# Kernel optimization log

Measured on AMD Instinct MI355X. Metric: run time of the kernel, lower is better.

Reference implementation:

```python
import jax, jax.numpy as jnp
import numpy as np
from jax import lax

B, P, S, H, F, V, O = 32, 24, 48, 512, 64, 50000, 16
EPS = 1e-5


def _lstm_scan(inputs, Wih, Whh, b):
    # inputs: [T, B, D]; PyTorch gate order i, f, g, o
    def step(carry, xt):
        h, c = carry
        g = xt @ Wih.T + h @ Whh.T + b
        i, f, gg, o = jnp.split(g, 4, axis=-1)
        c = jax.nn.sigmoid(f) * c + jax.nn.sigmoid(i) * jnp.tanh(gg)
        h = jax.nn.sigmoid(o) * jnp.tanh(c)
        return (h, c), h
    b_ = inputs.shape[1]
    h0 = jnp.zeros((b_, Whh.shape[1]), inputs.dtype)
    _, hs = lax.scan(step, (h0, h0), inputs)
    return hs


def setup_inputs() -> dict:
    key = jax.random.key(0)
    ks = jax.random.split(key, 16)
    x = jax.random.randint(ks[0], (B, P, S), 0, V)
    lens = jnp.sort(jax.random.randint(ks[1], (B,), 1, P + 1))[::-1]
    lens = lens.at[0].set(P)  # pack_padded: sorted desc, max len == P
    tok_len = jax.random.randint(ks[2], (B, P), 1, S + 1)
    tok_len = tok_len * (jnp.arange(P)[None, :] < lens[:, None])
    x_mask = jnp.arange(S)[None, None, :] >= tok_len[:, :, None]  # True = pad
    x_feature = jax.random.normal(ks[3], (B, P, S, F), dtype=jnp.float32)
    emb = jax.random.normal(ks[4], (V, H), dtype=jnp.float32) * 0.02
    w_attn = jax.random.normal(ks[5], (H,), dtype=jnp.float32) * 0.02
    b_attn = jnp.zeros((), jnp.float32)
    D = H + F
    s = 1.0 / np.sqrt(H)
    u = lambda k, sh: jax.random.uniform(k, sh, jnp.float32, -s, s)
    Wih_f, Whh_f = u(ks[6], (4 * H, D)), u(ks[7], (4 * H, H))
    bih_f, bhh_f = u(ks[8], (4 * H,)), u(ks[9], (4 * H,))
    Wih_b, Whh_b = u(ks[10], (4 * H, D)), u(ks[11], (4 * H, H))
    bih_b, bhh_b = u(ks[12], (4 * H,)), u(ks[13], (4 * H,))
    Wfc = u(ks[14], (O, 2 * H))
    bfc = jnp.zeros((O,), jnp.float32)
    gamma = jnp.ones((O,), jnp.float32)
    beta = jnp.zeros((O,), jnp.float32)
    return {"x": x, "x_mask": x_mask, "x_feature": x_feature,
            "sentences_len": lens, "clause": 0, "cls": 0,
            "emb": emb, "w_attn": w_attn, "b_attn": b_attn,
            "Wih_f": Wih_f, "Whh_f": Whh_f, "bih_f": bih_f, "bhh_f": bhh_f,
            "Wih_b": Wih_b, "Whh_b": Whh_b, "bih_b": bih_b, "bhh_b": bhh_b,
            "Wfc": Wfc, "bfc": bfc, "gamma": gamma, "beta": beta}


def reference(x, x_mask, x_feature, sentences_len, clause, cls,
              emb, w_attn, b_attn,
              Wih_f, Whh_f, bih_f, bhh_f,
              Wih_b, Whh_b, bih_b, bhh_b,
              Wfc, bfc, gamma, beta):
    # --- per-sentence embed + linear self-attention + masked sum pooling ---
    e = emb[x]                                             # [B,P,S,H]
    scores = jnp.einsum('bpsh,h->bps', e, w_attn) + b_attn  # [B,P,S]
    scores = jnp.where(x_mask, -1e30, scores)
    alpha = jax.nn.softmax(scores, axis=-1)
    alpha = jnp.where(x_mask, 0.0, alpha)                  # zeros empty sents; relu(softmax)=softmax
    valid = (~x_mask).astype(e.dtype)
    weighted = e * alpha[..., None]
    cat = jnp.concatenate([weighted, x_feature], axis=-1) * valid[..., None]
    rep = cat.sum(axis=2)                                  # [B,P,H+F]
    seq = jnp.transpose(rep, (1, 0, 2))                    # time-major [P,B,H+F]

    # --- packed bidirectional LSTM (per-sequence reversal for bwd dir) ---
    t = jnp.arange(P)[:, None]                             # [P,1]
    lens = sentences_len[None, :]                          # [1,B]
    valid_t = (t < lens)                                   # [P,B]
    h_fwd = _lstm_scan(seq, Wih_f, Whh_f, bih_f + bhh_f)
    rev_idx = jnp.clip(lens - 1 - t, 0)                    # [P,B]
    rev_in = jnp.take_along_axis(seq, rev_idx[..., None], axis=0)
    h_bwd_rev = _lstm_scan(rev_in, Wih_b, Whh_b, bih_b + bhh_b)
    h_bwd = jnp.take_along_axis(h_bwd_rev, rev_idx[..., None], axis=0)
    out_seq = jnp.concatenate([h_fwd, h_bwd], axis=-1) * valid_t[..., None]  # pad_packed zeros

    # --- tail: last timestep, fc, train-mode BN, relu, log_softmax(dim=0) ---
    last = out_seq[-1]                                     # [B,2H]
    z = jnp.reshape(last.T, (B, 2 * H))                    # faithful transpose+view quirk
    y = z @ Wfc.T + bfc                                    # [B,O]
    mean = y.mean(axis=0)
    var = y.var(axis=0)                                    # biased, as torch BN normalization
    y = gamma * (y - mean) / jnp.sqrt(var + EPS) + beta
    y = jax.nn.relu(y)
    return jax.nn.log_softmax(y, axis=0)
```

## Files before the change

### kernel.cpp

```cpp
#include <hip/hip_runtime.h>
#include <math.h>

#define BB_ 32
#define PP_ 24
#define SS_ 48
#define HH_ 512
#define FF_ 64
#define DD_ 576
#define G4_ 2048

typedef __attribute__((ext_vector_type(8))) short short8;
typedef __attribute__((ext_vector_type(4))) float f32x4;

__device__ __forceinline__ float sigf(float x) { return 1.f / (1.f + expf(-x)); }

__device__ __forceinline__ unsigned short f2bf(float f) {
    unsigned int u = __float_as_uint(f);
    u += 0x7FFFu + ((u >> 16) & 1u);
    return (unsigned short)(u >> 16);
}

__global__ void __launch_bounds__(256) prep_attn_kernel(
        const int* __restrict__ x, const unsigned int* __restrict__ maskw,
        const float* __restrict__ x_feature, const float* __restrict__ emb,
        const float* __restrict__ w_attn, const float* __restrict__ b_attn,
        const float* __restrict__ Whh, unsigned short* __restrict__ Bf,
        const float* __restrict__ Wih, unsigned short* __restrict__ Wbf,
        float* __restrict__ AfA, int* __restrict__ flags,
        float* __restrict__ seq, unsigned short* __restrict__ seqb)
{
    int blk = blockIdx.x, tid = threadIdx.x;
    if (blk < 768) {
        __shared__ float sc_s[SS_], alpha_s[SS_];
        __shared__ int vtok[SS_], vpos[SS_];
        __shared__ int nv_s, s_u8, s_f32;
        __shared__ int idx_s[SS_];
        __shared__ unsigned char msk_s[SS_];
        if (tid == 0) { s_u8 = 0; s_f32 = 0; }
        __syncthreads();
        int u8 = 0, f32 = 0;
        for (int i = tid; i < 9216; i += 256) {
            unsigned int w = maskw[i];
            if (w == 0x3F800000u) f32 = 1;
            else if (w > 1u) u8 = 1;
        }
        if (u8) s_u8 = 1;
        if (f32) s_f32 = 1;
        __syncthreads();
        int mode = s_f32 ? 2 : (s_u8 ? 1 : 0);
        int bp = blk, b = bp / PP_, p = bp % PP_;
        if (tid < SS_) {
            size_t i = (size_t)bp * SS_ + tid;
            idx_s[tid] = x[i];
            unsigned char mv;
            if (mode == 1)      mv = ((const unsigned char*)maskw)[i];
            else if (mode == 2) mv = (((const float*)maskw)[i] != 0.f);
            else                mv = (((const int*)maskw)[i] != 0);
            msk_s[tid] = mv;
        }
        __syncthreads();
        if (tid == 0) {
            int nv = 0;
            for (int s = 0; s < SS_; ++s)
                if (!msk_s[s]) { vtok[nv] = idx_s[s]; vpos[nv] = s; ++nv; }
            nv_s = nv;
        }
        __syncthreads();
        int nv = nv_s;
        int wave = tid >> 6, lane = tid & 63;
        float4 wa0 = ((const float4*)w_attn)[lane];
        float4 wa1 = ((const float4*)w_attn)[64 + lane];
        for (int j = wave; j < nv; j += 4) {
            const float4* er4 = (const float4*)(emb + (size_t)vtok[j] * HH_);
            float4 v0 = er4[lane], v1 = er4[64 + lane];
            float acc = v0.x * wa0.x + v0.y * wa0.y + v0.z * wa0.z + v0.w * wa0.w
                      + v1.x * wa1.x + v1.y * wa1.y + v1.z * wa1.z + v1.w * wa1.w;
            #pragma unroll
            for (int off = 32; off > 0; off >>= 1) acc += __shfl_down(acc, off, 64);
            if (lane == 0) sc_s[j] = acc + b_attn[0];
        }
        __syncthreads();
        if (tid == 0) {
            float m = -3.4e38f;
            for (int j = 0; j < nv; ++j) if (sc_s[j] > m) m = sc_s[j];
            float sum = 0.f;
            for (int j = 0; j < nv; ++j) { float a = expf(sc_s[j] - m); alpha_s[j] = a; sum += a; }
            float inv = (nv > 0) ? (1.f / sum) : 0.f;
            for (int j = 0; j < nv; ++j) alpha_s[j] *= inv;
        }
        __syncthreads();
        float acc0 = 0.f, acc1 = 0.f;
        for (int j = 0; j < nv; ++j) {
            float a = alpha_s[j];
            const float* er = emb + (size_t)vtok[j] * HH_;
            acc0 += a * er[tid];
            acc1 += a * er[tid + 256];
        }
        float* orow = seq + ((size_t)p * BB_ + b) * DD_;
        unsigned short* ob = seqb + ((size_t)p * BB_ + b) * DD_;
        orow[tid] = acc0;
        orow[tid + 256] = acc1;
        ob[tid] = f2bf(acc0);
        ob[tid + 256] = f2bf(acc1);
        if (tid < FF_) {
            float accF = 0.f;
            for (int j = 0; j < nv; ++j)
                accF += x_feature[((size_t)bp * SS_ + vpos[j]) * FF_ + tid];
            orow[HH_ + tid] = accF;
            ob[HH_ + tid] = f2bf(accF);
        }
    } else if (blk < 1280) {
        int idx = (blk - 768) * 256 + tid;
        int lane = idx & 63;
        int ks = (idx >> 6) & 15;
        int ti = (idx >> 10) & 1;
        int nb = idx >> 11;
        int c = lane & 15, q = lane >> 4;
        int nrow = (ti * 2 + (c >> 3)) * HH_ + nb * 8 + (c & 7);
        int k0 = ks * 32 + q * 8;
        const float* src = Whh + (size_t)nrow * HH_ + k0;
        unsigned int w0 = (unsigned int)f2bf(src[0]) | ((unsigned int)f2bf(src[1]) << 16);
        unsigned int w1 = (unsigned int)f2bf(src[2]) | ((unsigned int)f2bf(src[3]) << 16);
        unsigned int w2 = (unsigned int)f2bf(src[4]) | ((unsigned int)f2bf(src[5]) << 16);
        unsigned int w3 = (unsigned int)f2bf(src[6]) | ((unsigned int)f2bf(src[7]) << 16);
        *(uint4*)(Bf + (size_t)idx * 8) = make_uint4(w0, w1, w2, w3);
    } else if (blk < 2432) {
        int i = (blk - 1280) * 256 + tid;
        float4 v = ((const float4*)Wih)[i];
        ushort4 o;
        o.x = f2bf(v.x); o.y = f2bf(v.y); o.z = f2bf(v.z); o.w = f2bf(v.w);
        ((ushort4*)Wbf)[i] = o;
    } else if (blk < 2464) {
        int idx = (blk - 2432) * 256 + tid;
        if (idx < 8192) AfA[idx] = 0.f;
    } else {
        if (tid < 64) flags[tid] = 0;
    }
}

__global__ void __launch_bounds__(256) in_gates_mfma_kernel(
        const unsigned short* __restrict__ Ab,
        const unsigned short* __restrict__ Wbf,
        const float* __restrict__ bih,
        const float* __restrict__ bhh,
        float* __restrict__ Cout)
{
    int tid = threadIdx.x, lane = tid & 63, w = tid >> 6;
    int m0 = blockIdx.y * 16;
    int nb = blockIdx.x * 128 + w * 32;
    int c = lane & 15, q = lane >> 4;
    const unsigned short* Ap  = Ab  + (size_t)(m0 + c) * DD_ + q * 8;
    const unsigned short* Bp0 = Wbf + (size_t)(nb + c) * DD_ + q * 8;
    const unsigned short* Bp1 = Bp0 + 16 * DD_;
    f32x4 acc0 = {0.f, 0.f, 0.f, 0.f}, acc1 = {0.f, 0.f, 0.f, 0.f};
    for (int k = 0; k < DD_; k += 32) {
        short8 a  = *(const short8*)(Ap  + k);
        short8 b0 = *(const short8*)(Bp0 + k);
        short8 b1 = *(const short8*)(Bp1 + k);
        acc0 = __builtin_amdgcn_mfma_f32_16x16x32_bf16(a, b0, acc0, 0, 0, 0);
        acc1 = __builtin_amdgcn_mfma_f32_16x16x32_bf16(a, b1, acc1, 0, 0, 0);
    }
    #pragma unroll
    for (int r = 0; r < 4; ++r) {
        int m = m0 + q * 4 + r;
        int n0 = nb + c, n1 = nb + 16 + c;
        Cout[(size_t)m * G4_ + n0] = acc0[r] + bih[n0] + bhh[n0];
        Cout[(size_t)m * G4_ + n1] = acc1[r] + bih[n1] + bhh[n1];
    }
}

__global__ void __launch_bounds__(256) lstm_bwd_kernel(
        unsigned short* __restrict__ AfA, unsigned short* __restrict__ AfB,
        float* __restrict__ hbuf, const float* __restrict__ Ain,
        const unsigned short* __restrict__ Bfrag, int* __restrict__ flags,
        const float* __restrict__ seq, const int* __restrict__ lens,
        const float* __restrict__ Wih_b, const float* __restrict__ bih_b,
        const float* __restrict__ bhh_b, float* __restrict__ hbw)
{
    __shared__ float smem[19040];
    int tid = threadIdx.x;
    if (blockIdx.x < 64) {
        float* gl = smem;
        int lane = tid & 63, wv = tid >> 6;
        int mt = wv & 1, ti = wv >> 1;
        int nb = blockIdx.x;
        const short8* Bp = (const short8*)Bfrag + (((size_t)nb * 2 + ti) * 16) * 64 + lane;
        short8 bfr[16];
        #pragma unroll
        for (int ks = 0; ks < 16; ++ks) bfr[ks] = Bp[ks * 64];
        int c = lane & 15, q = lane >> 4;
        int g = ti * 2 + (c >> 3), ul = c & 7;
        int b2s = tid >> 1, hf2 = tid & 1;
        float creg[4] = {0.f, 0.f, 0.f, 0.f};
        const float* ainp = Ain + (size_t)(mt * 16 + q * 4) * G4_ + g * HH_ + nb * 8 + ul;
        float ainx[4], ainn[4];
        #pragma unroll
        for (int r = 0; r < 4; ++r) ainx[r] = ainp[(size_t)r * G4_];
        for (int t = 0; t < PP_; ++t) {
            if (t + 1 < PP_) {
                const float* np = ainp + (size_t)(t + 1) * BB_ * G4_;
                #pragma unroll
                for (int r = 0; r < 4; ++r) ainn[r] = np[(size_t)r * G4_];
            }
            const unsigned short* Af = (t & 1) ? AfB : AfA;
            unsigned short* An       = (t & 1) ? AfA : AfB;
            const unsigned long long* Ap64 =
                (const unsigned long long*)Af + ((size_t)(mt * 16) * 64 + lane) * 2;
            short8 a[16];
            #pragma unroll
            for (int ks = 0; ks < 16; ++ks) {
                unsigned long long lo = __hip_atomic_load(Ap64 + (size_t)ks * 128,
                        __ATOMIC_RELAXED, __HIP_MEMORY_SCOPE_AGENT);
                unsigned long long hi = __hip_atomic_load(Ap64 + (size_t)ks * 128 + 1,
                        __ATOMIC_RELAXED, __HIP_MEMORY_SCOPE_AGENT);
                union { unsigned long long u[2]; short8 s; } cv;
                cv.u[0] = lo; cv.u[1] = hi;
                a[ks] = cv.s;
            }
            f32x4 acA = {0.f,0.f,0.f,0.f}, acB = {0.f,0.f,0.f,0.f};
            f32x4 acC = {0.f,0.f,0.f,0.f}, acD = {0.f,0.f,0.f,0.f};
            #pragma unroll
            for (int ks = 0; ks < 16; ks += 4) {
                acA = __builtin_amdgcn_mfma_f32_16x16x32_bf16(a[ks],     bfr[ks],     acA, 0, 0, 0);
                acB = __builtin_amdgcn_mfma_f32_16x16x32_bf16(a[ks + 1], bfr[ks + 1], acB, 0, 0, 0);
                acC = __builtin_amdgcn_mfma_f32_16x16x32_bf16(a[ks + 2], bfr[ks + 2], acC, 0, 0, 0);
                acD = __builtin_amdgcn_mfma_f32_16x16x32_bf16(a[ks + 3], bfr[ks + 3], acD, 0, 0, 0);
            }
            #pragma unroll
            for (int r = 0; r < 4; ++r) {
                float v = (acA[r] + acB[r]) + (acC[r] + acD[r]) + ainx[r];
                v = (g == 2) ? tanhf(v) : sigf(v);
                gl[(g * 8 + ul) * 33 + (mt * 16 + q * 4 + r)] = v;
            }
            __syncthreads();
            if (t == PP_ - 1) {
                if (tid < 64) {
                    #pragma unroll
                    for (int uu = 0; uu < 4; ++uu) {
                        int u = hf2 * 4 + uu;
                        float iv = gl[(     u) * 33 + b2s];
                        float fv = gl[( 8 + u) * 33 + b2s];
                        float gv = gl[(16 + u) * 33 + b2s];
                        float ov = gl[(24 + u) * 33 + b2s];
                        creg[uu] = fv * creg[uu] + iv * gv;
                        hbuf[(size_t)b2s * HH_ + nb * 8 + u] = ov * tanhf(creg[uu]);
                    }
                }
            } else {
                if (tid < 64) {
                    float h4[4];
                    #pragma unroll
                    for (int uu = 0; uu < 4; ++uu) {
                        int u = hf2 * 4 + uu;
                        float iv = gl[(     u) * 33 + b2s];
                        float fv = gl[( 8 + u) * 33 + b2s];
                        float gv = gl[(16 + u) * 33 + b2s];
                        float ov = gl[(24 + u) * 33 + b2s];
                        creg[uu] = fv * creg[uu] + iv * gv;
                        h4[uu] = ov * tanhf(creg[uu]);
                    }
                    unsigned long long vv = (unsigned long long)f2bf(h4[0])
                                          | ((unsigned long long)f2bf(h4[1]) << 16)
                                          | ((unsigned long long)f2bf(h4[2]) << 32)
                                          | ((unsigned long long)f2bf(h4[3]) << 48);
                    size_t ub = ((((size_t)(b2s >> 4)) * 16 + (nb >> 2)) * 64
                                 + ((b2s & 15) + 16 * (nb & 3))) * 8 + hf2 * 4;
                    __hip_atomic_store((unsigned long long*)(AfA + (An - AfA) + ub), vv,
                                       __ATOMIC_RELAXED, __HIP_MEMORY_SCOPE_AGENT);
                    asm volatile("s_waitcnt vmcnt(0)" ::: "memory");
                    if (tid == 0)
                        __hip_atomic_store(&flags[nb], t + 1,
                                           __ATOMIC_RELAXED, __HIP_MEMORY_SCOPE_AGENT);
                    int target = t + 1;
                    while (true) {
                        int fvv = __hip_atomic_load(&flags[tid],
                                __ATOMIC_RELAXED, __HIP_MEMORY_SCOPE_AGENT);
                        if (__all(fvv >= target)) break;
                        __builtin_amdgcn_s_sleep(1);
                    }
                }
                __syncthreads();
            }
            #pragma unroll
            for (int r = 0; r < 4; ++r) ainx[r] = ainn[r];
        }
    } else {
        float* xsT = smem;
        int* pl = (int*)(smem + 19008);
        int blk2 = blockIdx.x - 64;
        if (tid < BB_) pl[tid] = lens[tid] - 1;
        __syncthreads();
        for (int idx = tid; idx < BB_ * DD_; idx += 256) {
            int b2 = idx / DD_;
            int k = idx - b2 * DD_;
            xsT[k * 33 + b2] = seq[((size_t)pl[b2] * BB_ + b2) * DD_ + k];
        }
        __syncthreads();
        int b = tid & 31, ul = tid >> 5;
        int u = blk2 * 8 + ul;
        const float* wi = Wih_b + (size_t)u * DD_;
        const float* wg = Wih_b + (size_t)(2 * HH_ + u) * DD_;
        const float* wo = Wih_b + (size_t)(3 * HH_ + u) * DD_;
        float gi = 0.f, gg = 0.f, go = 0.f;
        #pragma unroll 4
        for (int k = 0; k < DD_; k += 4) {
            float4 w1 = *(const float4*)(wi + k);
            float4 w2 = *(const float4*)(wg + k);
            float4 w3 = *(const float4*)(wo + k);
            float x0 = xsT[(k + 0) * 33 + b];
            float x1 = xsT[(k + 1) * 33 + b];
            float x2 = xsT[(k + 2) * 33 + b];
            float x3 = xsT[(k + 3) * 33 + b];
            gi += w1.x * x0 + w1.y * x1 + w1.z * x2 + w1.w * x3;
            gg += w2.x * x0 + w2.y * x1 + w2.z * x2 + w2.w * x3;
            go += w3.x * x0 + w3.y * x1 + w3.z * x2 + w3.w * x3;
        }
        gi += bih_b[u] + bhh_b[u];
        gg += bih_b[2 * HH_ + u] + bhh_b[2 * HH_ + u];
        go += bih_b[3 * HH_ + u] + bhh_b[3 * HH_ + u];
        float cc = sigf(gi) * tanhf(gg);
        hbw[(size_t)b * HH_ + u] = sigf(go) * tanhf(cc);
    }
}

__global__ void __launch_bounds__(1024) head_fused_kernel(
        const float* __restrict__ hf, const float* __restrict__ hbwd,
        const int* __restrict__ lens,
        const float* __restrict__ Wfc, const float* __restrict__ bfc,
        const float* __restrict__ gamma, const float* __restrict__ beta,
        float* __restrict__ out)
{
    __shared__ float tileL[32 * 1024];
    __shared__ float lmask[BB_];
    __shared__ float part[1024];
    __shared__ float ys[16][33];
    __shared__ float cstat[16];
    int tid = threadIdx.x;
    if (tid < BB_) lmask[tid] = (lens[tid] == PP_) ? 1.f : 0.f;
    __syncthreads();
    for (int j = tid; j < 32 * 1024; j += 1024) {
        int bb = j >> 10, col = j & 1023;
        float v = (col < HH_) ? hf[(size_t)bb * HH_ + col]
                              : hbwd[(size_t)bb * HH_ + col - HH_];
        tileL[j] = v * lmask[bb];
    }
    __syncthreads();
    int outi = tid & 511, half = tid >> 9;
    int i = outi >> 4, o = outi & 15;
    const float* wrow = Wfc + (size_t)o * 1024;
    float acc = 0.f;
    for (int q = 0; q < 32; ++q) {
        int j = i * 32 + q;
        #pragma unroll
        for (int bb2 = 0; bb2 < 16; ++bb2) {
            int bb = half * 16 + bb2;
            acc += tileL[bb * 1024 + j] * wrow[q * 32 + bb];
        }
    }
    part[tid] = acc;
    __syncthreads();
    if (tid < 512) ys[o][i] = part[tid] + part[tid + 512] + bfc[o];
    __syncthreads();
    if (tid < 16) {
        float mean = 0.f;
        for (int ii = 0; ii < 32; ++ii) mean += ys[tid][ii];
        mean *= (1.f / 32.f);
        float var = 0.f;
        for (int ii = 0; ii < 32; ++ii) { float d = ys[tid][ii] - mean; var += d * d; }
        var *= (1.f / 32.f);
        float inv = 1.f / sqrtf(var + 1e-5f);
        float gmm = gamma[tid], bt = beta[tid];
        float mx = -3.4e38f;
        for (int ii = 0; ii < 32; ++ii) {
            float v = gmm * (ys[tid][ii] - mean) * inv + bt;
            v = fmaxf(v, 0.f);
            ys[tid][ii] = v;
            mx = fmaxf(mx, v);
        }
        float s = 0.f;
        for (int ii = 0; ii < 32; ++ii) s += expf(ys[tid][ii] - mx);
        cstat[tid] = mx + logf(s);
    }
    __syncthreads();
    if (tid < 512) out[tid] = ys[o][i] - cstat[o];
}

extern "C" void kernel_launch(void* const* d_in, const int* in_sizes, int n_in,
                              void* d_out, int out_size, void* d_ws, size_t ws_size,
                              hipStream_t stream) {
    const int* x            = (const int*)d_in[0];
    const void* xm          = d_in[1];
    const float* x_feature  = (const float*)d_in[2];
    const int* lens         = (const int*)d_in[3];
    const float* emb    = (const float*)d_in[6];
    const float* w_attn = (const float*)d_in[7];
    const float* b_attn = (const float*)d_in[8];
    const float* Wih_f  = (const float*)d_in[9];
    const float* Whh_f  = (const float*)d_in[10];
    const float* bih_f  = (const float*)d_in[11];
    const float* bhh_f  = (const float*)d_in[12];
    const float* Wih_b  = (const float*)d_in[13];
    const float* bih_b  = (const float*)d_in[15];
    const float* bhh_b  = (const float*)d_in[16];
    const float* Wfc    = (const float*)d_in[17];
    const float* bfc    = (const float*)d_in[18];
    const float* gamma  = (const float*)d_in[19];
    const float* beta   = (const float*)d_in[20];

    float* ws    = (float*)d_ws;
    float* seq   = ws;
    float* Ain   = seq + (size_t)PP_ * BB_ * DD_;
    float* hb    = Ain + (size_t)PP_ * BB_ * G4_;
    float* hbuf  = hb + (size_t)BB_ * HH_;
    float* AfA   = hbuf + (size_t)BB_ * HH_;
    float* AfB   = AfA + 8192;
    float* Bfrag = AfB + 8192;
    float* Wbf   = Bfrag + 524288;
    int*  flags  = (int*)(Wbf + 589824);
    unsigned short* seqb = (unsigned short*)(Wbf + 589824 + 16);

    float* outp = (float*)d_out;

    prep_attn_kernel<<<dim3(2465), dim3(256), 0, stream>>>(
        x, (const unsigned int*)xm, x_feature, emb, w_attn, b_attn,
        Whh_f, (unsigned short*)Bfrag, Wih_f, (unsigned short*)Wbf,
        AfA, flags, seq, seqb);
    in_gates_mfma_kernel<<<dim3(16, 48), dim3(256), 0, stream>>>(
        seqb, (const unsigned short*)Wbf, bih_f, bhh_f, Ain);
    lstm_bwd_kernel<<<dim3(128), dim3(256), 0, stream>>>(
        (unsigned short*)AfA, (unsigned short*)AfB, hbuf, Ain,
        (const unsigned short*)Bfrag, flags,
        seq, lens, Wih_b, bih_b, bhh_b, hb);
    head_fused_kernel<<<dim3(1), dim3(1024), 0, stream>>>(
        hbuf, hb, lens, Wfc, bfc, gamma, beta, outp);
}
```

Baseline: 444.0 us.

## Replace global barrier with per-chunk flag polling in backward LSTM recurrence

The grid-wide spin barrier after each timestep is replaced. Each wave now polls producer flags and loads each K-chunk of the hidden state as soon as its four producer blocks have published, so the MMA inputs arrive incrementally instead of after all 64 blocks finish. The trailing __syncthreads is dropped and the next step's input-gate prefetch moves inline. This aims to cut barrier latency on the serial recurrence, at the cost of more polling traffic. Removing the block sync also risks the shared gate buffer being overwritten before it is consumed.

```diff
diff --git a/kernel.cpp b/kernel.cpp
--- a/kernel.cpp
+++ b/kernel.cpp
@@ -169,7 +169,7 @@
     }
 }
 
-__global__ void __launch_bounds__(256) lstm_bwd_kernel(
+__global__ void __launch_bounds__(256, 1) lstm_bwd_kernel(
         unsigned short* __restrict__ AfA, unsigned short* __restrict__ AfB,
         float* __restrict__ hbuf, const float* __restrict__ Ain,
         const unsigned short* __restrict__ Bfrag, int* __restrict__ flags,
@@ -193,29 +193,57 @@
         int b2s = tid >> 1, hf2 = tid & 1;
         float creg[4] = {0.f, 0.f, 0.f, 0.f};
         const float* ainp = Ain + (size_t)(mt * 16 + q * 4) * G4_ + g * HH_ + nb * 8 + ul;
-        float ainx[4], ainn[4];
-        #pragma unroll
-        for (int r = 0; r < 4; ++r) ainx[r] = ainp[(size_t)r * G4_];
         for (int t = 0; t < PP_; ++t) {
-            if (t + 1 < PP_) {
-                const float* np = ainp + (size_t)(t + 1) * BB_ * G4_;
+            float ainx[4];
+            {
+                const float* ap = ainp + (size_t)t * BB_ * G4_;
                 #pragma unroll
-                for (int r = 0; r < 4; ++r) ainn[r] = np[(size_t)r * G4_];
+                for (int r = 0; r < 4; ++r) ainx[r] = ap[(size_t)r * G4_];
             }
             const unsigned short* Af = (t & 1) ? AfB : AfA;
             unsigned short* An       = (t & 1) ? AfA : AfB;
             const unsigned long long* Ap64 =
                 (const unsigned long long*)Af + ((size_t)(mt * 16) * 64 + lane) * 2;
             short8 a[16];
-            #pragma unroll
-            for (int ks = 0; ks < 16; ++ks) {
-                unsigned long long lo = __hip_atomic_load(Ap64 + (size_t)ks * 128,
-                        __ATOMIC_RELAXED, __HIP_MEMORY_SCOPE_AGENT);
-                unsigned long long hi = __hip_atomic_load(Ap64 + (size_t)ks * 128 + 1,
-                        __ATOMIC_RELAXED, __HIP_MEMORY_SCOPE_AGENT);
-                union { unsigned long long u[2]; short8 s; } cv;
-                cv.u[0] = lo; cv.u[1] = hi;
-                a[ks] = cv.s;
+            if (t == 0) {
+                #pragma unroll
+                for (int ks = 0; ks < 16; ++ks) {
+                    unsigned long long lo = __hip_atomic_load(Ap64 + (size_t)ks * 128,
+                            __ATOMIC_RELAXED, __HIP_MEMORY_SCOPE_AGENT);
+                    unsigned long long hi = __hip_atomic_load(Ap64 + (size_t)ks * 128 + 1,
+                            __ATOMIC_RELAXED, __HIP_MEMORY_SCOPE_AGENT);
+                    union { unsigned long long u[2]; short8 s; } cv;
+                    cv.u[0] = lo; cv.u[1] = hi;
+                    a[ks] = cv.s;
+                }
+            } else {
+                unsigned int got = 0;
+                while (got != 0xFFFFu) {
+                    int fv = __hip_atomic_load(&flags[lane],
+                            __ATOMIC_RELAXED, __HIP_MEMORY_SCOPE_AGENT);
+                    unsigned long long bal = __ballot(fv >= t);
+                    unsigned int rdy = 0;
+                    #pragma unroll
+                    for (int ks = 0; ks < 16; ++ks)
+                        if (((bal >> (ks * 4)) & 0xFull) == 0xFull) rdy |= 1u << ks;
+                    unsigned int news = rdy & ~got;
+                    #pragma unroll
+                    for (int ks = 0; ks < 16; ++ks) {
+                        if (news & (1u << ks)) {
+                            unsigned long long lo = __hip_atomic_load(
+                                    Ap64 + (size_t)ks * 128,
+                                    __ATOMIC_RELAXED, __HIP_MEMORY_SCOPE_AGENT);
+                            unsigned long long hi = __hip_atomic_load(
+                                    Ap64 + (size_t)ks * 128 + 1,
+                                    __ATOMIC_RELAXED, __HIP_MEMORY_SCOPE_AGENT);
+                            union { unsigned long long u[2]; short8 s; } cv;
+                            cv.u[0] = lo; cv.u[1] = hi;
+                            a[ks] = cv.s;
+                        }
+                    }
+                    got |= news;
+                    if (got != 0xFFFFu) __builtin_amdgcn_s_sleep(1);
+                }
             }
             f32x4 acA = {0.f,0.f,0.f,0.f}, acB = {0.f,0.f,0.f,0.f};
             f32x4 acC = {0.f,0.f,0.f,0.f}, acD = {0.f,0.f,0.f,0.f};
@@ -265,24 +293,14 @@
                                           | ((unsigned long long)f2bf(h4[3]) << 48);
                     size_t ub = ((((size_t)(b2s >> 4)) * 16 + (nb >> 2)) * 64
                                  + ((b2s & 15) + 16 * (nb & 3))) * 8 + hf2 * 4;
-                    __hip_atomic_store((unsigned long long*)(AfA + (An - AfA) + ub), vv,
+                    __hip_atomic_store((unsigned long long*)(An + ub), vv,
                                        __ATOMIC_RELAXED, __HIP_MEMORY_SCOPE_AGENT);
                     asm volatile("s_waitcnt vmcnt(0)" ::: "memory");
                     if (tid == 0)
                         __hip_atomic_store(&flags[nb], t + 1,
                                            __ATOMIC_RELAXED, __HIP_MEMORY_SCOPE_AGENT);
-                    int target = t + 1;
-                    while (true) {
-                        int fvv = __hip_atomic_load(&flags[tid],
-                                __ATOMIC_RELAXED, __HIP_MEMORY_SCOPE_AGENT);
-                        if (__all(fvv >= target)) break;
-                        __builtin_amdgcn_s_sleep(1);
-                    }
                 }
-                __syncthreads();
             }
-            #pragma unroll
-            for (int r = 0; r < 4; ++r) ainx[r] = ainn[r];
         }
     } else {
         float* xsT = smem;
```

Result: no change. 445.1 us (+0.2%).

## Per-wave flag sync and shuffle-based LSTM cell update in forward recurrence

Applied to the files above, without the earlier changes.

Reorders the Whh fragment layout so each MFMA tile holds all four gates for four hidden units, which lets the cell update run entirely in registers via wave shuffles instead of going through an LDS gate buffer and a block-wide barrier. Cross-block synchronisation moves from one flag per block, with a single wave spinning, to one flag per wave (256 flags), and each wave waits only on the flags of its own batch half before reading h. The B fragments move from registers into LDS, and the input-gate loads are no longer prefetched one step ahead. The aim is to remove __syncthreads and the serial single-wave cell update from the per-step critical path, at the cost of more flag polling traffic and LDS reads inside the MFMA loop.

```diff
diff --git a/kernel.cpp b/kernel.cpp
--- a/kernel.cpp
+++ b/kernel.cpp
@@ -116,7 +116,7 @@
         int ti = (idx >> 10) & 1;
         int nb = idx >> 11;
         int c = lane & 15, q = lane >> 4;
-        int nrow = (ti * 2 + (c >> 3)) * HH_ + nb * 8 + (c & 7);
+        int nrow = (c >> 2) * HH_ + nb * 8 + ti * 4 + (c & 3);
         int k0 = ks * 32 + q * 8;
         const float* src = Whh + (size_t)nrow * HH_ + k0;
         unsigned int w0 = (unsigned int)f2bf(src[0]) | ((unsigned int)f2bf(src[1]) << 16);
@@ -134,7 +134,7 @@
         int idx = (blk - 2432) * 256 + tid;
         if (idx < 8192) AfA[idx] = 0.f;
     } else {
-        if (tid < 64) flags[tid] = 0;
+        flags[tid] = 0;
     }
 }
 
@@ -169,7 +169,7 @@
     }
 }
 
-__global__ void __launch_bounds__(256) lstm_bwd_kernel(
+__global__ void __launch_bounds__(256, 1) lstm_bwd_kernel(
         unsigned short* __restrict__ AfA, unsigned short* __restrict__ AfB,
         float* __restrict__ hbuf, const float* __restrict__ Ain,
         const unsigned short* __restrict__ Bfrag, int* __restrict__ flags,
@@ -177,35 +177,48 @@
         const float* __restrict__ Wih_b, const float* __restrict__ bih_b,
         const float* __restrict__ bhh_b, float* __restrict__ hbw)
 {
-    __shared__ float smem[19040];
+    __shared__ __align__(16) float smem[19040];
     int tid = threadIdx.x;
     if (blockIdx.x < 64) {
-        float* gl = smem;
         int lane = tid & 63, wv = tid >> 6;
         int mt = wv & 1, ti = wv >> 1;
         int nb = blockIdx.x;
-        const short8* Bp = (const short8*)Bfrag + (((size_t)nb * 2 + ti) * 16) * 64 + lane;
-        short8 bfr[16];
-        #pragma unroll
-        for (int ks = 0; ks < 16; ++ks) bfr[ks] = Bp[ks * 64];
         int c = lane & 15, q = lane >> 4;
-        int g = ti * 2 + (c >> 3), ul = c & 7;
-        int b2s = tid >> 1, hf2 = tid & 1;
+        int g = c >> 2, ul = c & 3;
+        short8* lsb = (short8*)smem + (size_t)wv * 1024 + lane;
+        {
+            const short8* Bg = (const short8*)Bfrag
+                             + ((size_t)(nb * 2 + ti) * 16) * 64 + lane;
+            #pragma unroll
+            for (int ks = 0; ks < 16; ++ks) lsb[ks * 64] = Bg[ks * 64];
+        }
+        int fid = mt * 128 + nb * 2 + ti;
+        int fb  = mt * 128;
+        int lsrc = lane & 51;
+        const float* ainp = Ain + (size_t)(mt * 16 + q * 4) * G4_
+                          + g * HH_ + nb * 8 + ti * 4 + ul;
         float creg[4] = {0.f, 0.f, 0.f, 0.f};
-        const float* ainp = Ain + (size_t)(mt * 16 + q * 4) * G4_ + g * HH_ + nb * 8 + ul;
-        float ainx[4], ainn[4];
-        #pragma unroll
-        for (int r = 0; r < 4; ++r) ainx[r] = ainp[(size_t)r * G4_];
         for (int t = 0; t < PP_; ++t) {
-            if (t + 1 < PP_) {
-                const float* np = ainp + (size_t)(t + 1) * BB_ * G4_;
+            float ainx[4];
+            {
+                const float* ap = ainp + (size_t)t * BB_ * G4_;
                 #pragma unroll
-                for (int r = 0; r < 4; ++r) ainn[r] = np[(size_t)r * G4_];
+                for (int r = 0; r < 4; ++r) ainx[r] = ap[(size_t)r * G4_];
+            }
+            if (t > 0) {
+                while (true) {
+                    int f0 = __hip_atomic_load(&flags[fb + lane],
+                            __ATOMIC_RELAXED, __HIP_MEMORY_SCOPE_AGENT);
+                    int f1 = __hip_atomic_load(&flags[fb + 64 + lane],
+                            __ATOMIC_RELAXED, __HIP_MEMORY_SCOPE_AGENT);
+                    if (__all(f0 >= t && f1 >= t)) break;
+                    __builtin_amdgcn_s_sleep(1);
+                }
             }
             const unsigned short* Af = (t & 1) ? AfB : AfA;
             unsigned short* An       = (t & 1) ? AfA : AfB;
             const unsigned long long* Ap64 =
-                (const unsigned long long*)Af + ((size_t)(mt * 16) * 64 + lane) * 2;
+                (const unsigned long long*)Af + (size_t)mt * 2048 + lane * 2;
             short8 a[16];
             #pragma unroll
             for (int ks = 0; ks < 16; ++ks) {
@@ -217,72 +230,63 @@
                 cv.u[0] = lo; cv.u[1] = hi;
                 a[ks] = cv.s;
             }
-            f32x4 acA = {0.f,0.f,0.f,0.f}, acB = {0.f,0.f,0.f,0.f};
-            f32x4 acC = {0.f,0.f,0.f,0.f}, acD = {0.f,0.f,0.f,0.f};
+            f32x4 ac0 = {0.f,0.f,0.f,0.f}, ac1 = {0.f,0.f,0.f,0.f};
+            f32x4 ac2 = {0.f,0.f,0.f,0.f}, ac3 = {0.f,0.f,0.f,0.f};
             #pragma unroll
             for (int ks = 0; ks < 16; ks += 4) {
-                acA = __builtin_amdgcn_mfma_f32_16x16x32_bf16(a[ks],     bfr[ks],     acA, 0, 0, 0);
-                acB = __builtin_amdgcn_mfma_f32_16x16x32_bf16(a[ks + 1], bfr[ks + 1], acB, 0, 0, 0);
-                acC = __builtin_amdgcn_mfma_f32_16x16x32_bf16(a[ks + 2], bfr[ks + 2], acC, 0, 0, 0);
-                acD = __builtin_amdgcn_mfma_f32_16x16x32_bf16(a[ks + 3], bfr[ks + 3], acD, 0, 0, 0);
-            }
+                ac0 = __builtin_amdgcn_mfma_f32_16x16x32_bf16(a[ks],     lsb[(ks    ) * 64], ac0, 0, 0, 0);
+                ac1 = __builtin_amdgcn_mfma_f32_16x16x32_bf16(a[ks + 1], lsb[(ks + 1) * 64], ac1, 0, 0, 0);
+                ac2 = __builtin_amdgcn_mfma_f32_16x16x32_bf16(a[ks + 2], lsb[(ks + 2) * 64], ac2, 0, 0, 0);
+                ac3 = __builtin_amdgcn_mfma_f32_16x16x32_bf16(a[ks + 3], lsb[(ks + 3) * 64], ac3, 0, 0, 0);
+            }
+            float vr[4];
             #pragma unroll
             for (int r = 0; r < 4; ++r) {
-                float v = (acA[r] + acB[r]) + (acC[r] + acD[r]) + ainx[r];
-                v = (g == 2) ? tanhf(v) : sigf(v);
-                gl[(g * 8 + ul) * 33 + (mt * 16 + q * 4 + r)] = v;
-            }
-            __syncthreads();
+                float xx = (ac0[r] + ac1[r]) + (ac2[r] + ac3[r]) + ainx[r];
+                float y  = (g == 2) ? (xx + xx) : xx;
+                float s  = 1.f / (1.f + expf(-y));
+                vr[r] = (g == 2) ? (s + s - 1.f) : s;
+            }
+            float ovsel = 0.f;
+            #pragma unroll
+            for (int r = 0; r < 4; ++r) {
+                float iv = __shfl(vr[r], lsrc,      64);
+                float fv = __shfl(vr[r], lsrc | 4,  64);
+                float gv = __shfl(vr[r], lsrc | 8,  64);
+                float ov = __shfl(vr[r], lsrc | 12, 64);
+                creg[r] = fv * creg[r] + iv * gv;
+                ovsel = (r == g) ? ov : ovsel;
+            }
+            float cg = (g == 0) ? creg[0] : (g == 1) ? creg[1]
+                     : (g == 2) ? creg[2] : creg[3];
+            float s2 = 1.f / (1.f + expf(-2.f * cg));
+            float hg = ovsel * (s2 + s2 - 1.f);
+            float h0 = __shfl(hg, (lane & 60),     64);
+            float h1 = __shfl(hg, (lane & 60) | 1, 64);
+            float h2 = __shfl(hg, (lane & 60) | 2, 64);
+            float h3 = __shfl(hg, (lane & 60) | 3, 64);
+            int b = mt * 16 + q * 4 + g;
             if (t == PP_ - 1) {
-                if (tid < 64) {
-                    #pragma unroll
-                    for (int uu = 0; uu < 4; ++uu) {
-                        int u = hf2 * 4 + uu;
-                        float iv = gl[(     u) * 33 + b2s];
-                        float fv = gl[( 8 + u) * 33 + b2s];
-                        float gv = gl[(16 + u) * 33 + b2s];
-                        float ov = gl[(24 + u) * 33 + b2s];
-                        creg[uu] = fv * creg[uu] + iv * gv;
-                        hbuf[(size_t)b2s * HH_ + nb * 8 + u] = ov * tanhf(creg[uu]);
-                    }
+                if (ul == 0) {
+                    *(float4*)(hbuf + (size_t)b * HH_ + nb * 8 + ti * 4) =
+                        make_float4(h0, h1, h2, h3);
                 }
             } else {
-                if (tid < 64) {
-                    float h4[4];
-                    #pragma unroll
-                    for (int uu = 0; uu < 4; ++uu) {
-                        int u = hf2 * 4 + uu;
-                        float iv = gl[(     u) * 33 + b2s];
-                        float fv = gl[( 8 + u) * 33 + b2s];
-                        float gv = gl[(16 + u) * 33 + b2s];
-                        float ov = gl[(24 + u) * 33 + b2s];
-                        creg[uu] = fv * creg[uu] + iv * gv;
-                        h4[uu] = ov * tanhf(creg[uu]);
-                    }
-                    unsigned long long vv = (unsigned long long)f2bf(h4[0])
-                                          | ((unsigned long long)f2bf(h4[1]) << 16)
-                                          | ((unsigned long long)f2bf(h4[2]) << 32)
-                                          | ((unsigned long long)f2bf(h4[3]) << 48);
-                    size_t ub = ((((size_t)(b2s >> 4)) * 16 + (nb >> 2)) * 64
-                                 + ((b2s & 15) + 16 * (nb & 3))) * 8 + hf2 * 4;
-                    __hip_atomic_store((unsigned long long*)(AfA + (An - AfA) + ub), vv,
+                if (ul == 0) {
+                    unsigned long long vv = (unsigned long long)f2bf(h0)
+                                          | ((unsigned long long)f2bf(h1) << 16)
+                                          | ((unsigned long long)f2bf(h2) << 32)
+                                          | ((unsigned long long)f2bf(h3) << 48);
+                    size_t ui = ((size_t)(mt * 16 + (nb >> 2)) * 64
+                                 + (q * 4 + g) + 16 * (nb & 3)) * 2 + ti;
+                    __hip_atomic_store((unsigned long long*)An + ui, vv,
                                        __ATOMIC_RELAXED, __HIP_MEMORY_SCOPE_AGENT);
-                    asm volatile("s_waitcnt vmcnt(0)" ::: "memory");
-                    if (tid == 0)
-                        __hip_atomic_store(&flags[nb], t + 1,
-                                           __ATOMIC_RELAXED, __HIP_MEMORY_SCOPE_AGENT);
-                    int target = t + 1;
-                    while (true) {
-                        int fvv = __hip_atomic_load(&flags[tid],
-                                __ATOMIC_RELAXED, __HIP_MEMORY_SCOPE_AGENT);
-                        if (__all(fvv >= target)) break;
-                        __builtin_amdgcn_s_sleep(1);
-                    }
                 }
-                __syncthreads();
-            }
-            #pragma unroll
-            for (int r = 0; r < 4; ++r) ainx[r] = ainn[r];
+                asm volatile("s_waitcnt vmcnt(0)" ::: "memory");
+                if (lane == 0)
+                    __hip_atomic_store(&flags[fid], t + 1,
+                                       __ATOMIC_RELAXED, __HIP_MEMORY_SCOPE_AGENT);
+            }
         }
     } else {
         float* xsT = smem;
@@ -417,7 +421,7 @@
     float* Bfrag = AfB + 8192;
     float* Wbf   = Bfrag + 524288;
     int*  flags  = (int*)(Wbf + 589824);
-    unsigned short* seqb = (unsigned short*)(Wbf + 589824 + 16);
+    unsigned short* seqb = (unsigned short*)(Wbf + 589824 + 256);
 
     float* outp = (float*)d_out;
 
```

Result: slower. 453.2 us (+2.1%).

## Replace flag barrier with per-element step-tagged hidden state in persistent LSTM

Applied to the files above, without the earlier changes.

The recurrent LSTM kernel no longer uses a global flag array and all-blocks spin barrier each timestep. Every bf16 hidden value is now stored with a 16-bit timestep tag in a 32-bit word, and consumers poll their own A-fragment words until all tags match the current step. Cell updates are spread across all 256 threads instead of 64, and the gate buffer is double-buffered in shared memory to drop the trailing syncthreads. This trades the barrier round trip for twice the hidden-state traffic and repeated polling loads.

```diff
diff --git a/kernel.cpp b/kernel.cpp
--- a/kernel.cpp
+++ b/kernel.cpp
@@ -26,7 +26,7 @@
         const float* __restrict__ w_attn, const float* __restrict__ b_attn,
         const float* __restrict__ Whh, unsigned short* __restrict__ Bf,
         const float* __restrict__ Wih, unsigned short* __restrict__ Wbf,
-        float* __restrict__ AfA, int* __restrict__ flags,
+        unsigned int* __restrict__ AfAt,
         float* __restrict__ seq, unsigned short* __restrict__ seqb)
 {
     int blk = blockIdx.x, tid = threadIdx.x;
@@ -130,11 +130,9 @@
         ushort4 o;
         o.x = f2bf(v.x); o.y = f2bf(v.y); o.z = f2bf(v.z); o.w = f2bf(v.w);
         ((ushort4*)Wbf)[i] = o;
-    } else if (blk < 2464) {
+    } else {
         int idx = (blk - 2432) * 256 + tid;
-        if (idx < 8192) AfA[idx] = 0.f;
-    } else {
-        if (tid < 64) flags[tid] = 0;
+        ((uint4*)AfAt)[idx] = make_uint4(0u, 0u, 0u, 0u);
     }
 }
 
@@ -169,15 +167,15 @@
     }
 }
 
-__global__ void __launch_bounds__(256) lstm_bwd_kernel(
-        unsigned short* __restrict__ AfA, unsigned short* __restrict__ AfB,
+__global__ void __launch_bounds__(256, 1) lstm_bwd_kernel(
+        unsigned int* __restrict__ AfAt, unsigned int* __restrict__ AfBt,
         float* __restrict__ hbuf, const float* __restrict__ Ain,
-        const unsigned short* __restrict__ Bfrag, int* __restrict__ flags,
+        const unsigned short* __restrict__ Bfrag,
         const float* __restrict__ seq, const int* __restrict__ lens,
         const float* __restrict__ Wih_b, const float* __restrict__ bih_b,
         const float* __restrict__ bhh_b, float* __restrict__ hbw)
 {
-    __shared__ float smem[19040];
+    __shared__ __align__(16) float smem[19040];
     int tid = threadIdx.x;
     if (blockIdx.x < 64) {
         float* gl = smem;
@@ -190,32 +188,60 @@
         for (int ks = 0; ks < 16; ++ks) bfr[ks] = Bp[ks * 64];
         int c = lane & 15, q = lane >> 4;
         int g = ti * 2 + (c >> 3), ul = c & 7;
-        int b2s = tid >> 1, hf2 = tid & 1;
-        float creg[4] = {0.f, 0.f, 0.f, 0.f};
-        const float* ainp = Ain + (size_t)(mt * 16 + q * 4) * G4_ + g * HH_ + nb * 8 + ul;
-        float ainx[4], ainn[4];
-        #pragma unroll
-        for (int r = 0; r < 4; ++r) ainx[r] = ainp[(size_t)r * G4_];
+        int eb = tid >> 3, eu = tid & 7;
+        float creg = 0.f;
+        size_t eidx = ((((size_t)(eb >> 4)) * 16 + (nb >> 2)) * 64
+                       + ((eb & 15) + 16 * (nb & 3))) * 8 + eu;
+        const float* ainp = Ain + (size_t)(mt * 16 + q * 4) * G4_
+                          + g * HH_ + nb * 8 + ul;
         for (int t = 0; t < PP_; ++t) {
-            if (t + 1 < PP_) {
-                const float* np = ainp + (size_t)(t + 1) * BB_ * G4_;
+            float ainx[4];
+            {
+                const float* ap = ainp + (size_t)t * BB_ * G4_;
                 #pragma unroll
-                for (int r = 0; r < 4; ++r) ainn[r] = np[(size_t)r * G4_];
-            }
-            const unsigned short* Af = (t & 1) ? AfB : AfA;
-            unsigned short* An       = (t & 1) ? AfA : AfB;
-            const unsigned long long* Ap64 =
-                (const unsigned long long*)Af + ((size_t)(mt * 16) * 64 + lane) * 2;
+                for (int r = 0; r < 4; ++r) ainx[r] = ap[(size_t)r * G4_];
+            }
+            unsigned tgt = (unsigned)t;
+            const unsigned long long* Bas =
+                (const unsigned long long*)((t & 1) ? AfBt : AfAt)
+                + (size_t)mt * 4096 + lane * 4;
+            while (true) {
+                unsigned ok = 1u;
+                #pragma unroll
+                for (int ks = 0; ks < 16; ++ks) {
+                    unsigned long long d = __hip_atomic_load(Bas + (size_t)ks * 256,
+                            __ATOMIC_RELAXED, __HIP_MEMORY_SCOPE_AGENT);
+                    ok &= (((unsigned)d & 0xFFFFu) == tgt)
+                        & (((unsigned)(d >> 32) & 0xFFFFu) == tgt);
+                }
+                if (__all(ok)) break;
+                __builtin_amdgcn_s_sleep(1);
+            }
             short8 a[16];
-            #pragma unroll
-            for (int ks = 0; ks < 16; ++ks) {
-                unsigned long long lo = __hip_atomic_load(Ap64 + (size_t)ks * 128,
-                        __ATOMIC_RELAXED, __HIP_MEMORY_SCOPE_AGENT);
-                unsigned long long hi = __hip_atomic_load(Ap64 + (size_t)ks * 128 + 1,
-                        __ATOMIC_RELAXED, __HIP_MEMORY_SCOPE_AGENT);
-                union { unsigned long long u[2]; short8 s; } cv;
-                cv.u[0] = lo; cv.u[1] = hi;
-                a[ks] = cv.s;
+            while (true) {
+                unsigned ok = 1u;
+                #pragma unroll
+                for (int ks = 0; ks < 16; ++ks) {
+                    const unsigned long long* p = Bas + (size_t)ks * 256;
+                    unsigned long long d0 = __hip_atomic_load(p,
+                            __ATOMIC_RELAXED, __HIP_MEMORY_SCOPE_AGENT);
+                    unsigned long long d1 = __hip_atomic_load(p + 1,
+                            __ATOMIC_RELAXED, __HIP_MEMORY_SCOPE_AGENT);
+                    unsigned long long d2 = __hip_atomic_load(p + 2,
+                            __ATOMIC_RELAXED, __HIP_MEMORY_SCOPE_AGENT);
+                    unsigned long long d3 = __hip_atomic_load(p + 3,
+                            __ATOMIC_RELAXED, __HIP_MEMORY_SCOPE_AGENT);
+                    ok &= (((unsigned)d0 & 0xFFFFu) == tgt) & (((unsigned)(d0 >> 32) & 0xFFFFu) == tgt)
+                        & (((unsigned)d1 & 0xFFFFu) == tgt) & (((unsigned)(d1 >> 32) & 0xFFFFu) == tgt)
+                        & (((unsigned)d2 & 0xFFFFu) == tgt) & (((unsigned)(d2 >> 32) & 0xFFFFu) == tgt)
+                        & (((unsigned)d3 & 0xFFFFu) == tgt) & (((unsigned)(d3 >> 32) & 0xFFFFu) == tgt);
+                    a[ks][0] = (short)(d0 >> 16); a[ks][1] = (short)(d0 >> 48);
+                    a[ks][2] = (short)(d1 >> 16); a[ks][3] = (short)(d1 >> 48);
+                    a[ks][4] = (short)(d2 >> 16); a[ks][5] = (short)(d2 >> 48);
+                    a[ks][6] = (short)(d3 >> 16); a[ks][7] = (short)(d3 >> 48);
+                }
+                if (__all(ok)) break;
+                __builtin_amdgcn_s_sleep(1);
             }
             f32x4 acA = {0.f,0.f,0.f,0.f}, acB = {0.f,0.f,0.f,0.f};
             f32x4 acC = {0.f,0.f,0.f,0.f}, acD = {0.f,0.f,0.f,0.f};
@@ -226,63 +252,28 @@
                 acC = __builtin_amdgcn_mfma_f32_16x16x32_bf16(a[ks + 2], bfr[ks + 2], acC, 0, 0, 0);
                 acD = __builtin_amdgcn_mfma_f32_16x16x32_bf16(a[ks + 3], bfr[ks + 3], acD, 0, 0, 0);
             }
+            float* gls = gl + (t & 1) * 1056;
             #pragma unroll
             for (int r = 0; r < 4; ++r) {
                 float v = (acA[r] + acB[r]) + (acC[r] + acD[r]) + ainx[r];
                 v = (g == 2) ? tanhf(v) : sigf(v);
-                gl[(g * 8 + ul) * 33 + (mt * 16 + q * 4 + r)] = v;
+                gls[(g * 8 + ul) * 33 + (mt * 16 + q * 4 + r)] = v;
             }
             __syncthreads();
+            float iv = gls[(     eu) * 33 + eb];
+            float fv = gls[( 8 + eu) * 33 + eb];
+            float gv = gls[(16 + eu) * 33 + eb];
+            float ov = gls[(24 + eu) * 33 + eb];
+            creg = fv * creg + iv * gv;
+            float h = ov * tanhf(creg);
             if (t == PP_ - 1) {
-                if (tid < 64) {
-                    #pragma unroll
-                    for (int uu = 0; uu < 4; ++uu) {
-                        int u = hf2 * 4 + uu;
-                        float iv = gl[(     u) * 33 + b2s];
-                        float fv = gl[( 8 + u) * 33 + b2s];
-                        float gv = gl[(16 + u) * 33 + b2s];
-                        float ov = gl[(24 + u) * 33 + b2s];
-                        creg[uu] = fv * creg[uu] + iv * gv;
-                        hbuf[(size_t)b2s * HH_ + nb * 8 + u] = ov * tanhf(creg[uu]);
-                    }
-                }
+                hbuf[(size_t)eb * HH_ + nb * 8 + eu] = h;
             } else {
-                if (tid < 64) {
-                    float h4[4];
-                    #pragma unroll
-                    for (int uu = 0; uu < 4; ++uu) {
-                        int u = hf2 * 4 + uu;
-                        float iv = gl[(     u) * 33 + b2s];
-                        float fv = gl[( 8 + u) * 33 + b2s];
-                        float gv = gl[(16 + u) * 33 + b2s];
-                        float ov = gl[(24 + u) * 33 + b2s];
-                        creg[uu] = fv * creg[uu] + iv * gv;
-                        h4[uu] = ov * tanhf(creg[uu]);
-                    }
-                    unsigned long long vv = (unsigned long long)f2bf(h4[0])
-                                          | ((unsigned long long)f2bf(h4[1]) << 16)
-                                          | ((unsigned long long)f2bf(h4[2]) << 32)
-                                          | ((unsigned long long)f2bf(h4[3]) << 48);
-                    size_t ub = ((((size_t)(b2s >> 4)) * 16 + (nb >> 2)) * 64
-                                 + ((b2s & 15) + 16 * (nb & 3))) * 8 + hf2 * 4;
-                    __hip_atomic_store((unsigned long long*)(AfA + (An - AfA) + ub), vv,
-                                       __ATOMIC_RELAXED, __HIP_MEMORY_SCOPE_AGENT);
-                    asm volatile("s_waitcnt vmcnt(0)" ::: "memory");
-                    if (tid == 0)
-                        __hip_atomic_store(&flags[nb], t + 1,
-                                           __ATOMIC_RELAXED, __HIP_MEMORY_SCOPE_AGENT);
-                    int target = t + 1;
-                    while (true) {
-                        int fvv = __hip_atomic_load(&flags[tid],
-                                __ATOMIC_RELAXED, __HIP_MEMORY_SCOPE_AGENT);
-                        if (__all(fvv >= target)) break;
-                        __builtin_amdgcn_s_sleep(1);
-                    }
-                }
-                __syncthreads();
-            }
-            #pragma unroll
-            for (int r = 0; r < 4; ++r) ainx[r] = ainn[r];
+                unsigned w = ((unsigned)f2bf(h) << 16) | (unsigned)(t + 1);
+                unsigned int* Ant = (t & 1) ? AfAt : AfBt;
+                __hip_atomic_store(Ant + eidx, w,
+                                   __ATOMIC_RELAXED, __HIP_MEMORY_SCOPE_AGENT);
+            }
         }
     } else {
         float* xsT = smem;
@@ -412,24 +403,23 @@
     float* Ain   = seq + (size_t)PP_ * BB_ * DD_;
     float* hb    = Ain + (size_t)PP_ * BB_ * G4_;
     float* hbuf  = hb + (size_t)BB_ * HH_;
-    float* AfA   = hbuf + (size_t)BB_ * HH_;
-    float* AfB   = AfA + 8192;
-    float* Bfrag = AfB + 8192;
+    unsigned int* AfAt = (unsigned int*)(hbuf + (size_t)BB_ * HH_);
+    unsigned int* AfBt = AfAt + 16384;
+    float* Bfrag = (float*)(AfBt + 16384);
     float* Wbf   = Bfrag + 524288;
-    int*  flags  = (int*)(Wbf + 589824);
-    unsigned short* seqb = (unsigned short*)(Wbf + 589824 + 16);
+    unsigned short* seqb = (unsigned short*)(Wbf + 589824);
 
     float* outp = (float*)d_out;
 
-    prep_attn_kernel<<<dim3(2465), dim3(256), 0, stream>>>(
+    prep_attn_kernel<<<dim3(2464), dim3(256), 0, stream>>>(
         x, (const unsigned int*)xm, x_feature, emb, w_attn, b_attn,
         Whh_f, (unsigned short*)Bfrag, Wih_f, (unsigned short*)Wbf,
-        AfA, flags, seq, seqb);
+        AfAt, seq, seqb);
     in_gates_mfma_kernel<<<dim3(16, 48), dim3(256), 0, stream>>>(
         seqb, (const unsigned short*)Wbf, bih_f, bhh_f, Ain);
     lstm_bwd_kernel<<<dim3(128), dim3(256), 0, stream>>>(
-        (unsigned short*)AfA, (unsigned short*)AfB, hbuf, Ain,
-        (const unsigned short*)Bfrag, flags,
+        AfAt, AfBt, hbuf, Ain,
+        (const unsigned short*)Bfrag,
         seq, lens, Wih_b, bih_b, bhh_b, hb);
     head_fused_kernel<<<dim3(1), dim3(1024), 0, stream>>>(
         hbuf, hb, lens, Wfc, bfc, gamma, beta, outp);
```

Measured after the change: 463.2 us. 1.04x slower.
